# Performance work log

Measured on AMD Instinct MI355X. Metric: run time of the kernel, lower is better.

## Reference

```python
import jax, jax.numpy as jnp
import numpy as np

N_NODES = 50000
N_EDGES = 800000
IN_DIM = 128
HIDDEN = 32
HEADS = 4
OUT_DIM = 64
NEG_SLOPE = 0.2  # PyG GATConv default


def setup_inputs() -> dict:
    key = jax.random.key(0)
    ks = jax.random.split(key, 12)
    s = 0.05
    return {
        "x": jax.random.normal(ks[0], (N_NODES, IN_DIM), dtype=jnp.float32),
        "edge_index": jax.random.randint(ks[1], (2, N_EDGES), 0, N_NODES, dtype=jnp.int64),
        # layer 1: out = HEADS * HIDDEN, concat=True
        "W1": jax.random.normal(ks[2], (IN_DIM, HEADS * HIDDEN), dtype=jnp.float32) * s,
        "a_src1": jax.random.normal(ks[3], (HEADS, HIDDEN), dtype=jnp.float32) * s,
        "a_dst1": jax.random.normal(ks[4], (HEADS, HIDDEN), dtype=jnp.float32) * s,
        "b1": jnp.zeros((HEADS * HIDDEN,), dtype=jnp.float32),
        # layer 2: heads=1, concat=False
        "W2": jax.random.normal(ks[5], (HEADS * HIDDEN, OUT_DIM), dtype=jnp.float32) * s,
        "a_src2": jax.random.normal(ks[6], (1, OUT_DIM), dtype=jnp.float32) * s,
        "a_dst2": jax.random.normal(ks[7], (1, OUT_DIM), dtype=jnp.float32) * s,
        "b2": jnp.zeros((OUT_DIM,), dtype=jnp.float32),
    }


def _gat_conv(x, src, dst, W, a_src, a_dst, b, heads, concat):
    """PyG-style GATConv. src/dst already include self-loops."""
    N = x.shape[0]
    C = W.shape[1] // heads
    h = (x @ W).reshape(N, heads, C)              # [N,H,C]
    al_s = jnp.sum(h * a_src, axis=-1)            # [N,H]
    al_d = jnp.sum(h * a_dst, axis=-1)            # [N,H]
    e = jax.nn.leaky_relu(al_s[src] + al_d[dst], NEG_SLOPE)  # [E,H]
    # numerically-stable segment softmax over incoming edges of each dst node
    m = jax.ops.segment_max(e, dst, num_segments=N)          # [N,H]
    ex = jnp.exp(e - m[dst])
    denom = jax.ops.segment_sum(ex, dst, num_segments=N)     # [N,H]
    alpha = ex / denom[dst]                                   # [E,H]
    out = jax.ops.segment_sum(h[src] * alpha[:, :, None], dst, num_segments=N)  # [N,H,C]
    out = out.reshape(N, heads * C) if concat else out.mean(axis=1)
    return out + b


def reference(x, edge_index, W1, a_src1, a_dst1, b1, W2, a_src2, a_dst2, b2):
    N = x.shape[0]
    loop = jnp.arange(N, dtype=edge_index.dtype)
    src = jnp.concatenate([edge_index[0], loop])
    dst = jnp.concatenate([edge_index[1], loop])
    h = jax.nn.relu(_gat_conv(x, src, dst, W1, a_src1, a_dst1, b1, HEADS, True))
    out = _gat_conv(h, src, dst, W2, a_src2, a_dst2, b2, 1, False)
    return jax.nn.log_softmax(out, axis=1)
```

## Files before the change

kernel.cpp:

```cpp
#include <hip/hip_runtime.h>
#include <hip/hip_bf16.h>
#include <math.h>

#define N_NODES 50000
#define N_EDGES 800000
#define E_TOT   (N_EDGES + N_NODES)
#define IN_DIM  128
#define HID     128
#define ODIM    64
#define NEG     0.2f
#define NB1     ((N_NODES + 255) / 256)
#define NCHUNK  ((N_NODES + 31) / 32)
#define NREP    8

typedef short bf16x8 __attribute__((ext_vector_type(8)));
typedef float f32x4 __attribute__((ext_vector_type(4)));
typedef float f32x2 __attribute__((ext_vector_type(2)));
typedef unsigned short ushort_t;

__device__ __forceinline__ float lrelu(float x) { return x >= 0.f ? x : NEG * x; }

__device__ __forceinline__ unsigned short f2b(float v) {
  unsigned int b = __float_as_uint(v);
  b += 0x7fffu + ((b >> 16) & 1u);
  return (unsigned short)(b >> 16);
}
__device__ __forceinline__ float b2f(unsigned short u) {
  return __uint_as_float(((unsigned int)u) << 16);
}
__device__ __forceinline__ unsigned int f2b2(float lo, float hi) {
  union { __hip_bfloat162 h; unsigned int u; } cv;
  cv.h = __float22bfloat162_rn(make_float2(lo, hi));
  return cv.u;
}
__device__ __forceinline__ float blo(unsigned int v) { return __uint_as_float(v << 16); }
__device__ __forceinline__ float bhi(unsigned int v) { return __uint_as_float(v & 0xffff0000u); }

__device__ __forceinline__ f32x2 f8x2lo(unsigned int v) {
  return __builtin_amdgcn_cvt_pk_f32_fp8((int)v, false);
}
__device__ __forceinline__ f32x2 f8x2hi(unsigned int v) {
  return __builtin_amdgcn_cvt_pk_f32_fp8((int)v, true);
}
__device__ __forceinline__ unsigned char f2f8(float v) {
  return (unsigned char)(__builtin_amdgcn_cvt_pk_fp8_f32(v, v, 0, false) & 0xff);
}

__global__ void k_detect(const void* ei, int* flag) {
  if (threadIdx.x == 0 && blockIdx.x == 0) {
    const int* p = (const int*)ei;
    int allz = 1;
    for (int i = 0; i < 64; ++i) if (p[2 * i + 1] != 0) { allz = 0; break; }
    *flag = allz;
  }
}

__device__ __forceinline__ int e_src(const void* ei, int f, int e) {
  if (e >= N_EDGES) return e - N_EDGES;
  return f ? (int)((const long long*)ei)[e] : ((const int*)ei)[e];
}
__device__ __forceinline__ int e_dst(const void* ei, int f, int e) {
  if (e >= N_EDGES) return e - N_EDGES;
  return f ? (int)((const long long*)ei)[N_EDGES + e] : ((const int*)ei)[N_EDGES + e];
}

__global__ void k_hist(const void* ei, const int* flag, int* degr, int* rank) {
  int e = blockIdx.x * 256 + threadIdx.x;
  if (e >= E_TOT) return;
  int r = blockIdx.x & (NREP - 1);
  int d = e_dst(ei, *flag, e);
  rank[e] = atomicAdd(&degr[r * N_NODES + d], 1);
}

__global__ void k_scan1(const int* __restrict__ degr, int* __restrict__ offs, int* __restrict__ bsums) {
  __shared__ int sm[256];
  int t = threadIdx.x, i = blockIdx.x * 256 + t;
  int v = 0;
  if (i < N_NODES) {
    #pragma unroll
    for (int r = 0; r < NREP; ++r) v += degr[r * N_NODES + i];
  }
  sm[t] = v;
  __syncthreads();
  for (int o = 1; o < 256; o <<= 1) {
    int add = (t >= o) ? sm[t - o] : 0;
    __syncthreads();
    sm[t] += add;
    __syncthreads();
  }
  if (i < N_NODES) offs[i] = sm[t] - v;
  if (t == 255) bsums[blockIdx.x] = sm[255];
}

__global__ void k_scan2(int* bsums) {
  __shared__ int sm[256];
  int t = threadIdx.x;
  int v = (t < NB1) ? bsums[t] : 0;
  sm[t] = v;
  __syncthreads();
  for (int o = 1; o < 256; o <<= 1) {
    int add = (t >= o) ? sm[t - o] : 0;
    __syncthreads();
    sm[t] += add;
    __syncthreads();
  }
  if (t < NB1) bsums[t] = sm[t] - v;
}

__global__ void k_scan3(int* __restrict__ offs, const int* __restrict__ bsums,
                        const int* __restrict__ degr, int* __restrict__ repbase) {
  int i = blockIdx.x * 256 + threadIdx.x;
  if (i < N_NODES) {
    int o = offs[i] + bsums[blockIdx.x];
    offs[i] = o;
    int run = o;
    #pragma unroll
    for (int r = 0; r < NREP; ++r) {
      repbase[r * N_NODES + i] = run;
      run += degr[r * N_NODES + i];
    }
  }
  if (i == 0) offs[N_NODES] = E_TOT;
}

__global__ void k_scatter(const void* ei, const int* __restrict__ flag,
                          const int* __restrict__ repbase,
                          const int* __restrict__ rank, int* __restrict__ srcs) {
  int e = blockIdx.x * 256 + threadIdx.x;
  if (e >= E_TOT) return;
  int f = *flag;
  int d = e_dst(ei, f, e);
  int r = blockIdx.x & (NREP - 1);
  srcs[repbase[r * N_NODES + d] + rank[e]] = e_src(ei, f, e);
}

__global__ void k_prep(const float* __restrict__ W1, const float* __restrict__ W2,
                       ushort_t* __restrict__ Wt1, ushort_t* __restrict__ Wt2) {
  int i = blockIdx.x * 256 + threadIdx.x;
  if (i < 128 * 128) { int k = i >> 7, n = i & 127; Wt1[n * 128 + k] = f2b(W1[i]); }
  if (i < 128 * 64)  { int k = i >> 6, n = i & 63;  Wt2[n * 128 + k] = f2b(W2[i]); }
}

__global__ __launch_bounds__(256) void k_mm1(const float* __restrict__ x,
                                             const ushort_t* __restrict__ Wt,
                                             ushort_t* __restrict__ h1b,
                                             unsigned char* __restrict__ h1f8) {
  __shared__ ushort_t xs[32 * 128];
  int t = threadIdx.x;
  int w = t >> 6, l = t & 63;
  int lr = l & 15, lk = l >> 4;
  int nodeSub = (w & 1) * 16, colBase = (w >> 1) * 64;
  bf16x8 bfrag[4][4];
  #pragma unroll
  for (int ct = 0; ct < 4; ++ct)
    #pragma unroll
    for (int ks = 0; ks < 4; ++ks) {
      int n = colBase + ct * 16 + lr;
      int k = ks * 32 + lk * 8;
      bfrag[ct][ks] = *(const bf16x8*)&Wt[n * 128 + k];
    }
  int rr = t >> 3, c0 = (t & 7) * 16;
  for (int chunk = blockIdx.x; chunk < NCHUNK; chunk += gridDim.x) {
    int base = chunk * 32;
    int srcRow = base + rr; if (srcRow >= N_NODES) srcRow = N_NODES - 1;
    const float4* xr = (const float4*)&x[(size_t)srcRow * IN_DIM + c0];
    float4 f0 = xr[0], f1 = xr[1], f2 = xr[2], f3 = xr[3];
    uint4 w0, w1;
    w0.x = f2b2(f0.x, f0.y); w0.y = f2b2(f0.z, f0.w);
    w0.z = f2b2(f1.x, f1.y); w0.w = f2b2(f1.z, f1.w);
    w1.x = f2b2(f2.x, f2.y); w1.y = f2b2(f2.z, f2.w);
    w1.z = f2b2(f3.x, f3.y); w1.w = f2b2(f3.z, f3.w);
    char* xsb = (char*)xs;
    int swz = (rr & 7) << 4;
    *(uint4*)(xsb + rr * 256 + ((c0 * 2 +  0) ^ swz)) = w0;
    *(uint4*)(xsb + rr * 256 + ((c0 * 2 + 16) ^ swz)) = w1;
    __syncthreads();
    f32x4 acc[4] = {{0,0,0,0},{0,0,0,0},{0,0,0,0},{0,0,0,0}};
    int arow = nodeSub + lr;
    #pragma unroll
    for (int ks = 0; ks < 4; ++ks) {
      bf16x8 a = *(const bf16x8*)((const char*)xs + arow * 256 +
                                  ((ks * 64 + lk * 16) ^ ((arow & 7) << 4)));
      #pragma unroll
      for (int ct = 0; ct < 4; ++ct)
        acc[ct] = __builtin_amdgcn_mfma_f32_16x16x32_bf16(a, bfrag[ct][ks], acc[ct], 0, 0, 0);
    }
    __syncthreads();
    #pragma unroll
    for (int ct = 0; ct < 4; ++ct)
      #pragma unroll
      for (int r = 0; r < 4; ++r) {
        int node = base + nodeSub + lk * 4 + r;
        if (node < N_NODES) {
          float v = acc[ct][r];
          int col = colBase + ct * 16 + lr;
          h1b[(size_t)node * HID + col] = f2b(v);
          h1f8[(size_t)node * HID + col] = f2f8(v);
        }
      }
  }
}

__global__ __launch_bounds__(256) void k_mm2(const ushort_t* __restrict__ xb,
                                             const ushort_t* __restrict__ Wt,
                                             ushort_t* __restrict__ h2b,
                                             unsigned char* __restrict__ h2f8) {
  __shared__ ushort_t xs[32 * 128];
  int t = threadIdx.x;
  int w = t >> 6, l = t & 63;
  int lr = l & 15, lk = l >> 4;
  int nodeSub = (w & 1) * 16, colBase = (w >> 1) * 32;
  bf16x8 bfrag[2][4];
  #pragma unroll
  for (int ct = 0; ct < 2; ++ct)
    #pragma unroll
    for (int ks = 0; ks < 4; ++ks) {
      int n = colBase + ct * 16 + lr;
      int k = ks * 32 + lk * 8;
      bfrag[ct][ks] = *(const bf16x8*)&Wt[n * 128 + k];
    }
  int rr = t >> 3, c0 = (t & 7) * 16;
  for (int chunk = blockIdx.x; chunk < NCHUNK; chunk += gridDim.x) {
    int base = chunk * 32;
    int srcRow = base + rr; if (srcRow >= N_NODES) srcRow = N_NODES - 1;
    const uint4* xr = (const uint4*)&xb[(size_t)srcRow * HID + c0];
    uint4 w0 = xr[0], w1 = xr[1];
    char* xsb = (char*)xs;
    int swz = (rr & 7) << 4;
    *(uint4*)(xsb + rr * 256 + ((c0 * 2 +  0) ^ swz)) = w0;
    *(uint4*)(xsb + rr * 256 + ((c0 * 2 + 16) ^ swz)) = w1;
    __syncthreads();
    f32x4 acc[2] = {{0,0,0,0},{0,0,0,0}};
    int arow = nodeSub + lr;
    #pragma unroll
    for (int ks = 0; ks < 4; ++ks) {
      bf16x8 a = *(const bf16x8*)((const char*)xs + arow * 256 +
                                  ((ks * 64 + lk * 16) ^ ((arow & 7) << 4)));
      #pragma unroll
      for (int ct = 0; ct < 2; ++ct)
        acc[ct] = __builtin_amdgcn_mfma_f32_16x16x32_bf16(a, bfrag[ct][ks], acc[ct], 0, 0, 0);
    }
    __syncthreads();
    #pragma unroll
    for (int ct = 0; ct < 2; ++ct)
      #pragma unroll
      for (int r = 0; r < 4; ++r) {
        int node = base + nodeSub + lk * 4 + r;
        if (node < N_NODES) {
          float v = acc[ct][r];
          int col = colBase + ct * 16 + lr;
          h2b[(size_t)node * ODIM + col] = f2b(v);
          h2f8[(size_t)node * ODIM + col] = f2f8(v);
        }
      }
  }
}

__global__ __launch_bounds__(256) void k_al1(const ushort_t* __restrict__ h1b,
                                             const float* __restrict__ asrc,
                                             const float* __restrict__ adst, float* __restrict__ als,
                                             float* __restrict__ ald) {
  int t = threadIdx.x;
  int n = blockIdx.x * 16 + (t >> 4);
  int c8 = (t & 15) * 8;
  uint4 v = *(const uint4*)&h1b[(size_t)n * HID + c8];
  float4 a0 = *(const float4*)&asrc[c8], a1 = *(const float4*)&asrc[c8 + 4];
  float4 d0 = *(const float4*)&adst[c8], d1 = *(const float4*)&adst[c8 + 4];
  float f0 = blo(v.x), f1 = bhi(v.x), f2 = blo(v.y), f3 = bhi(v.y);
  float f4 = blo(v.z), f5 = bhi(v.z), f6 = blo(v.w), f7 = bhi(v.w);
  float s = f0*a0.x + f1*a0.y + f2*a0.z + f3*a0.w + f4*a1.x + f5*a1.y + f6*a1.z + f7*a1.w;
  float d = f0*d0.x + f1*d0.y + f2*d0.z + f3*d0.w + f4*d1.x + f5*d1.y + f6*d1.z + f7*d1.w;
  s += __shfl_xor(s, 1); s += __shfl_xor(s, 2);
  d += __shfl_xor(d, 1); d += __shfl_xor(d, 2);
  if ((t & 3) == 0) {
    int head = (t & 15) >> 2;
    als[n * 4 + head] = s;
    ald[n * 4 + head] = d;
  }
}

__global__ __launch_bounds__(256) void k_al2(const ushort_t* __restrict__ h2b,
                                             const float* __restrict__ asrc,
                                             const float* __restrict__ adst, float* __restrict__ als,
                                             float* __restrict__ ald) {
  int t = threadIdx.x;
  int n = blockIdx.x * 32 + (t >> 3);
  if (n >= N_NODES) return;
  int c8 = (t & 7) * 8;
  uint4 v = *(const uint4*)&h2b[(size_t)n * ODIM + c8];
  float4 a0 = *(const float4*)&asrc[c8], a1 = *(const float4*)&asrc[c8 + 4];
  float4 d0 = *(const float4*)&adst[c8], d1 = *(const float4*)&adst[c8 + 4];
  float f0 = blo(v.x), f1 = bhi(v.x), f2 = blo(v.y), f3 = bhi(v.y);
  float f4 = blo(v.z), f5 = bhi(v.z), f6 = blo(v.w), f7 = bhi(v.w);
  float s = f0*a0.x + f1*a0.y + f2*a0.z + f3*a0.w + f4*a1.x + f5*a1.y + f6*a1.z + f7*a1.w;
  float d = f0*d0.x + f1*d0.y + f2*d0.z + f3*d0.w + f4*d1.x + f5*d1.y + f6*d1.z + f7*d1.w;
  s += __shfl_xor(s, 1); s += __shfl_xor(s, 2); s += __shfl_xor(s, 4);
  d += __shfl_xor(d, 1); d += __shfl_xor(d, 2); d += __shfl_xor(d, 4);
  if ((t & 7) == 0) { als[n] = s; ald[n] = d; }
}

__global__ __launch_bounds__(256) void k_agg1(const unsigned char* __restrict__ h1f8,
                                              const float* __restrict__ als,
                                              const float* __restrict__ ald, const int* __restrict__ offs,
                                              const int* __restrict__ srcs, const float* __restrict__ b1,
                                              ushort_t* __restrict__ out1b) {
  int t = threadIdx.x;
  int w = t >> 6, l = t & 63;
  int eg = l >> 4, cl = l & 15, head = cl >> 2;
  int n = blockIdx.x * 4 + w;
  int off0 = offs[n], deg = offs[n + 1] - off0;
  const float4* als4 = (const float4*)als;
  float4 ad = ((const float4*)ald)[n];
  const unsigned char* hb = h1f8 + cl * 8;

  float ds = 0.f;
  float num0 = 0, num1 = 0, num2 = 0, num3 = 0, num4 = 0, num5 = 0, num6 = 0, num7 = 0;

  for (int cbase = 0; cbase < deg; cbase += 64) {
    int j0 = cbase + l;
    float w0 = 0.f, w1 = 0.f, w2 = 0.f, w3 = 0.f;
    int sb = 0;
    if (j0 < deg) {
      int s = srcs[off0 + j0];
      sb = s << 7;
      float4 a = als4[s];
      w0 = __expf(lrelu(a.x + ad.x)); w1 = __expf(lrelu(a.y + ad.y));
      w2 = __expf(lrelu(a.z + ad.z)); w3 = __expf(lrelu(a.w + ad.w));
    }
    int pw01 = (int)f2b2(w0, w1), pw23 = (int)f2b2(w2, w3);
    int cn = (deg - cbase) < 64 ? (deg - cbase) : 64;
    for (int jj = 0; jj < cn; jj += 8) {
      int jA = jj + eg, jB = jj + 4 + eg;
      int boA = __shfl(sb, jA), boB = __shfl(sb, jB);
      uint2 vA = *(const uint2*)(hb + boA);
      uint2 vB = *(const uint2*)(hb + boB);
      unsigned int uA01 = (unsigned int)__shfl(pw01, jA);
      unsigned int uA23 = (unsigned int)__shfl(pw23, jA);
      unsigned int uB01 = (unsigned int)__shfl(pw01, jB);
      unsigned int uB23 = (unsigned int)__shfl(pw23, jB);
      unsigned int upA = head < 2 ? uA01 : uA23;
      unsigned int upB = head < 2 ? uB01 : uB23;
      float wA = (head & 1) ? bhi(upA) : blo(upA);
      float wB = (head & 1) ? bhi(upB) : blo(upB);
      ds += wA + wB;
      f32x2 p0 = f8x2lo(vA.x), p1 = f8x2hi(vA.x);
      f32x2 p2 = f8x2lo(vA.y), p3 = f8x2hi(vA.y);
      num0 = fmaf(wA, p0.x, num0); num1 = fmaf(wA, p0.y, num1);
      num2 = fmaf(wA, p1.x, num2); num3 = fmaf(wA, p1.y, num3);
      num4 = fmaf(wA, p2.x, num4); num5 = fmaf(wA, p2.y, num5);
      num6 = fmaf(wA, p3.x, num6); num7 = fmaf(wA, p3.y, num7);
      p0 = f8x2lo(vB.x); p1 = f8x2hi(vB.x);
      p2 = f8x2lo(vB.y); p3 = f8x2hi(vB.y);
      num0 = fmaf(wB, p0.x, num0); num1 = fmaf(wB, p0.y, num1);
      num2 = fmaf(wB, p1.x, num2); num3 = fmaf(wB, p1.y, num3);
      num4 = fmaf(wB, p2.x, num4); num5 = fmaf(wB, p2.y, num5);
      num6 = fmaf(wB, p3.x, num6); num7 = fmaf(wB, p3.y, num7);
    }
  }
  #pragma unroll
  for (int o = 16; o <= 32; o <<= 1) {
    num0 += __shfl_xor(num0, o); num1 += __shfl_xor(num1, o);
    num2 += __shfl_xor(num2, o); num3 += __shfl_xor(num3, o);
    num4 += __shfl_xor(num4, o); num5 += __shfl_xor(num5, o);
    num6 += __shfl_xor(num6, o); num7 += __shfl_xor(num7, o);
    ds += __shfl_xor(ds, o);
  }
  if (l < 16) {
    float rd = 1.f / ds;
    int c8 = cl * 8;
    float4 bb0 = *(const float4*)&b1[c8];
    float4 bb1 = *(const float4*)&b1[c8 + 4];
    float o0 = fmaxf(num0 * rd + bb0.x, 0.f);
    float o1 = fmaxf(num1 * rd + bb0.y, 0.f);
    float o2 = fmaxf(num2 * rd + bb0.z, 0.f);
    float o3 = fmaxf(num3 * rd + bb0.w, 0.f);
    float o4 = fmaxf(num4 * rd + bb1.x, 0.f);
    float o5 = fmaxf(num5 * rd + bb1.y, 0.f);
    float o6 = fmaxf(num6 * rd + bb1.z, 0.f);
    float o7 = fmaxf(num7 * rd + bb1.w, 0.f);
    uint4 pk;
    pk.x = f2b2(o0, o1); pk.y = f2b2(o2, o3);
    pk.z = f2b2(o4, o5); pk.w = f2b2(o6, o7);
    *(uint4*)&out1b[(size_t)n * HID + c8] = pk;
  }
}

__global__ __launch_bounds__(256) void k_agg2(const unsigned char* __restrict__ h2f8,
                                              const float* __restrict__ als,
                                              const float* __restrict__ ald, const int* __restrict__ offs,
                                              const int* __restrict__ srcs, const float* __restrict__ b2,
                                              float* __restrict__ out) {
  int t = threadIdx.x;
  int w = t >> 6, l = t & 63;
  int eg = l >> 3, cl = l & 7;
  int n = blockIdx.x * 4 + w;
  int off0 = offs[n], deg = offs[n + 1] - off0;
  float adv = ald[n];
  const unsigned char* hb = h2f8 + cl * 8;

  float ds = 0.f;
  float num0 = 0, num1 = 0, num2 = 0, num3 = 0, num4 = 0, num5 = 0, num6 = 0, num7 = 0;

  for (int cbase = 0; cbase < deg; cbase += 64) {
    int j0 = cbase + l;
    float wv = 0.f;
    int sb = 0;
    if (j0 < deg) {
      int s = srcs[off0 + j0];
      sb = s << 6;
      wv = __expf(lrelu(als[s] + adv));
    }
    int cn = (deg - cbase) < 64 ? (deg - cbase) : 64;
    for (int jj = 0; jj < cn; jj += 16) {
      int jA = jj + eg, jB = jj + 8 + eg;
      int boA = __shfl(sb, jA), boB = __shfl(sb, jB);
      uint2 vA = *(const uint2*)(hb + boA);
      uint2 vB = *(const uint2*)(hb + boB);
      float wA = __shfl(wv, jA), wB = __shfl(wv, jB);
      ds += wA + wB;
      f32x2 p0 = f8x2lo(vA.x), p1 = f8x2hi(vA.x);
      f32x2 p2 = f8x2lo(vA.y), p3 = f8x2hi(vA.y);
      num0 = fmaf(wA, p0.x, num0); num1 = fmaf(wA, p0.y, num1);
      num2 = fmaf(wA, p1.x, num2); num3 = fmaf(wA, p1.y, num3);
      num4 = fmaf(wA, p2.x, num4); num5 = fmaf(wA, p2.y, num5);
      num6 = fmaf(wA, p3.x, num6); num7 = fmaf(wA, p3.y, num7);
      p0 = f8x2lo(vB.x); p1 = f8x2hi(vB.x);
      p2 = f8x2lo(vB.y); p3 = f8x2hi(vB.y);
      num0 = fmaf(wB, p0.x, num0); num1 = fmaf(wB, p0.y, num1);
      num2 = fmaf(wB, p1.x, num2); num3 = fmaf(wB, p1.y, num3);
      num4 = fmaf(wB, p2.x, num4); num5 = fmaf(wB, p2.y, num5);
      num6 = fmaf(wB, p3.x, num6); num7 = fmaf(wB, p3.y, num7);
    }
  }
  #pragma unroll
  for (int o = 8; o <= 32; o <<= 1) {
    num0 += __shfl_xor(num0, o); num1 += __shfl_xor(num1, o);
    num2 += __shfl_xor(num2, o); num3 += __shfl_xor(num3, o);
    num4 += __shfl_xor(num4, o); num5 += __shfl_xor(num5, o);
    num6 += __shfl_xor(num6, o); num7 += __shfl_xor(num7, o);
    ds += __shfl_xor(ds, o);
  }
  if (l < 8) {
    float rd = 1.f / ds;
    int c8 = cl * 8;
    float4 bb0 = *(const float4*)&b2[c8];
    float4 bb1 = *(const float4*)&b2[c8 + 4];
    float v0 = num0 * rd + bb0.x, v1 = num1 * rd + bb0.y;
    float v2 = num2 * rd + bb0.z, v3 = num3 * rd + bb0.w;
    float v4 = num4 * rd + bb1.x, v5 = num5 * rd + bb1.y;
    float v6 = num6 * rd + bb1.z, v7 = num7 * rd + bb1.w;
    float mx = fmaxf(fmaxf(fmaxf(v0, v1), fmaxf(v2, v3)), fmaxf(fmaxf(v4, v5), fmaxf(v6, v7)));
    #pragma unroll
    for (int o = 1; o <= 4; o <<= 1) mx = fmaxf(mx, __shfl_xor(mx, o));
    float sum = __expf(v0 - mx) + __expf(v1 - mx) + __expf(v2 - mx) + __expf(v3 - mx)
              + __expf(v4 - mx) + __expf(v5 - mx) + __expf(v6 - mx) + __expf(v7 - mx);
    #pragma unroll
    for (int o = 1; o <= 4; o <<= 1) sum += __shfl_xor(sum, o);
    float ls = __logf(sum);
    float4 r0, r1;
    r0.x = (v0 - mx) - ls; r0.y = (v1 - mx) - ls; r0.z = (v2 - mx) - ls; r0.w = (v3 - mx) - ls;
    r1.x = (v4 - mx) - ls; r1.y = (v5 - mx) - ls; r1.z = (v6 - mx) - ls; r1.w = (v7 - mx) - ls;
    *(float4*)&out[(size_t)n * ODIM + c8] = r0;
    *(float4*)&out[(size_t)n * ODIM + c8 + 4] = r1;
  }
}

extern "C" void kernel_launch(void* const* d_in, const int* in_sizes, int n_in,
                              void* d_out, int out_size, void* d_ws, size_t ws_size,
                              hipStream_t stream) {
  const float* x   = (const float*)d_in[0];
  const void*  ei  = d_in[1];
  const float* W1  = (const float*)d_in[2];
  const float* as1 = (const float*)d_in[3];
  const float* ad1 = (const float*)d_in[4];
  const float* b1  = (const float*)d_in[5];
  const float* W2  = (const float*)d_in[6];
  const float* as2 = (const float*)d_in[7];
  const float* ad2 = (const float*)d_in[8];
  const float* b2  = (const float*)d_in[9];
  float* out = (float*)d_out;

  char* ws = (char*)d_ws;
  size_t o = 0;
  auto alloc = [&](size_t bytes) { void* p = (void*)(ws + o); o += (bytes + 255) & ~(size_t)255; return p; };
  ushort_t* h1b   = (ushort_t*)alloc((size_t)N_NODES * HID * 2);
  ushort_t* out1b = (ushort_t*)alloc((size_t)N_NODES * HID * 2);
  ushort_t* h2b   = (ushort_t*)alloc((size_t)N_NODES * ODIM * 2);
  unsigned char* h1f8 = (unsigned char*)alloc((size_t)N_NODES * HID);
  ushort_t* Wt1   = (ushort_t*)alloc((size_t)128 * 128 * 2);
  ushort_t* Wt2   = (ushort_t*)alloc((size_t)64 * 128 * 2);
  float* als1 = (float*)alloc((size_t)N_NODES * 4 * 4);
  float* ald1 = (float*)alloc((size_t)N_NODES * 4 * 4);
  float* als2 = (float*)alloc((size_t)N_NODES * 4);
  float* ald2 = (float*)alloc((size_t)N_NODES * 4);
  int*   degr = (int*)alloc((size_t)NREP * N_NODES * 4);
  int*   repbase = (int*)alloc((size_t)NREP * N_NODES * 4);
  int*   offs = (int*)alloc((size_t)(N_NODES + 1) * 4);
  int*   rank = (int*)alloc((size_t)E_TOT * 4);
  int*   srcs = (int*)alloc((size_t)E_TOT * 4);
  int*   bsums= (int*)alloc((size_t)NB1 * 4);
  int*   flag = (int*)alloc(4);
  unsigned char* h2f8 = (unsigned char*)rank;

  hipMemsetAsync(degr, 0, (size_t)NREP * N_NODES * 4, stream);
  k_detect<<<1, 64, 0, stream>>>(ei, flag);

  int egrid = (E_TOT + 255) / 256;
  k_hist   <<<egrid, 256, 0, stream>>>(ei, flag, degr, rank);
  k_scan1  <<<NB1,   256, 0, stream>>>(degr, offs, bsums);
  k_scan2  <<<1,     256, 0, stream>>>(bsums);
  k_scan3  <<<NB1,   256, 0, stream>>>(offs, bsums, degr, repbase);
  k_scatter<<<egrid, 256, 0, stream>>>(ei, flag, repbase, rank, srcs);
  k_prep   <<<64,    256, 0, stream>>>(W1, W2, Wt1, Wt2);

  k_mm1  <<<512, 256, 0, stream>>>(x, Wt1, h1b, h1f8);
  k_al1  <<<N_NODES / 16, 256, 0, stream>>>(h1b, as1, ad1, als1, ald1);
  k_agg1 <<<(N_NODES + 3) / 4, 256, 0, stream>>>(h1f8, als1, ald1, offs, srcs, b1, out1b);

  k_mm2  <<<512, 256, 0, stream>>>(out1b, Wt2, h2b, h2f8);
  k_al2  <<<(N_NODES + 31) / 32, 256, 0, stream>>>(h2b, as2, ad2, als2, ald2);
  k_agg2 <<<(N_NODES + 3) / 4, 256, 0, stream>>>(h2f8, als2, ald2, offs, srcs, b2, out);
}
```

Before: 148.6 us.

## Map two nodes per wavefront in aggregation kernels and fold detect into prep

Both edge-aggregation kernels now give each destination node a 32-lane half-wave instead of a full 64-lane wave. Edge chunks are therefore 32 wide and the shuffles are offset into the matching half. The aim is to stop wasting lanes on low-degree nodes, since average degree is about 17, and to halve the block count. The separate int32/int64 index-detect kernel is merged into k_prep as an extra block, saving one launch and moving weight prep earlier. The trade-off is fewer lanes in flight per edge for high-degree nodes, so more loop iterations there.

```diff
diff --git a/kernel.cpp b/kernel.cpp
--- a/kernel.cpp
+++ b/kernel.cpp
@@ -46,15 +46,6 @@
   return (unsigned char)(__builtin_amdgcn_cvt_pk_fp8_f32(v, v, 0, false) & 0xff);
 }
 
-__global__ void k_detect(const void* ei, int* flag) {
-  if (threadIdx.x == 0 && blockIdx.x == 0) {
-    const int* p = (const int*)ei;
-    int allz = 1;
-    for (int i = 0; i < 64; ++i) if (p[2 * i + 1] != 0) { allz = 0; break; }
-    *flag = allz;
-  }
-}
-
 __device__ __forceinline__ int e_src(const void* ei, int f, int e) {
   if (e >= N_EDGES) return e - N_EDGES;
   return f ? (int)((const long long*)ei)[e] : ((const int*)ei)[e];
@@ -62,6 +53,23 @@
 __device__ __forceinline__ int e_dst(const void* ei, int f, int e) {
   if (e >= N_EDGES) return e - N_EDGES;
   return f ? (int)((const long long*)ei)[N_EDGES + e] : ((const int*)ei)[N_EDGES + e];
+}
+
+__global__ void k_prep(const float* __restrict__ W1, const float* __restrict__ W2,
+                       ushort_t* __restrict__ Wt1, ushort_t* __restrict__ Wt2,
+                       const void* ei, int* flag) {
+  if (blockIdx.x == 64) {
+    if (threadIdx.x == 0) {
+      const int* p = (const int*)ei;
+      int allz = 1;
+      for (int i = 0; i < 64; ++i) if (p[2 * i + 1] != 0) { allz = 0; break; }
+      *flag = allz;
+    }
+    return;
+  }
+  int i = blockIdx.x * 256 + threadIdx.x;
+  if (i < 128 * 128) { int k = i >> 7, n = i & 127; Wt1[n * 128 + k] = f2b(W1[i]); }
+  if (i < 128 * 64)  { int k = i >> 6, n = i & 63;  Wt2[n * 128 + k] = f2b(W2[i]); }
 }
 
 __global__ void k_hist(const void* ei, const int* flag, int* degr, int* rank) {
@@ -132,13 +140,6 @@
   int d = e_dst(ei, f, e);
   int r = blockIdx.x & (NREP - 1);
   srcs[repbase[r * N_NODES + d] + rank[e]] = e_src(ei, f, e);
-}
-
-__global__ void k_prep(const float* __restrict__ W1, const float* __restrict__ W2,
-                       ushort_t* __restrict__ Wt1, ushort_t* __restrict__ Wt2) {
-  int i = blockIdx.x * 256 + threadIdx.x;
-  if (i < 128 * 128) { int k = i >> 7, n = i & 127; Wt1[n * 128 + k] = f2b(W1[i]); }
-  if (i < 128 * 64)  { int k = i >> 6, n = i & 63;  Wt2[n * 128 + k] = f2b(W2[i]); }
 }
 
 __global__ __launch_bounds__(256) void k_mm1(const float* __restrict__ x,
@@ -306,8 +307,10 @@
                                               ushort_t* __restrict__ out1b) {
   int t = threadIdx.x;
   int w = t >> 6, l = t & 63;
-  int eg = l >> 4, cl = l & 15, head = cl >> 2;
-  int n = blockIdx.x * 4 + w;
+  int hw = l >> 5, lh = l & 31;
+  int sg = lh >> 4, cl = lh & 15, head = cl >> 2;
+  int lbase = hw << 5;
+  int n = blockIdx.x * 8 + w * 2 + hw;
   int off0 = offs[n], deg = offs[n + 1] - off0;
   const float4* als4 = (const float4*)als;
   float4 ad = ((const float4*)ald)[n];
@@ -316,8 +319,8 @@
   float ds = 0.f;
   float num0 = 0, num1 = 0, num2 = 0, num3 = 0, num4 = 0, num5 = 0, num6 = 0, num7 = 0;
 
-  for (int cbase = 0; cbase < deg; cbase += 64) {
-    int j0 = cbase + l;
+  for (int cbase = 0; cbase < deg; cbase += 32) {
+    int j0 = cbase + lh;
     float w0 = 0.f, w1 = 0.f, w2 = 0.f, w3 = 0.f;
     int sb = 0;
     if (j0 < deg) {
@@ -328,16 +331,16 @@
       w2 = __expf(lrelu(a.z + ad.z)); w3 = __expf(lrelu(a.w + ad.w));
     }
     int pw01 = (int)f2b2(w0, w1), pw23 = (int)f2b2(w2, w3);
-    int cn = (deg - cbase) < 64 ? (deg - cbase) : 64;
-    for (int jj = 0; jj < cn; jj += 8) {
-      int jA = jj + eg, jB = jj + 4 + eg;
-      int boA = __shfl(sb, jA), boB = __shfl(sb, jB);
+    int cn = (deg - cbase) < 32 ? (deg - cbase) : 32;
+    for (int jj = 0; jj < cn; jj += 4) {
+      int jA = jj + sg, jB = jj + 2 + sg;
+      int boA = __shfl(sb, lbase + jA), boB = __shfl(sb, lbase + jB);
       uint2 vA = *(const uint2*)(hb + boA);
       uint2 vB = *(const uint2*)(hb + boB);
-      unsigned int uA01 = (unsigned int)__shfl(pw01, jA);
-      unsigned int uA23 = (unsigned int)__shfl(pw23, jA);
-      unsigned int uB01 = (unsigned int)__shfl(pw01, jB);
-      unsigned int uB23 = (unsigned int)__shfl(pw23, jB);
+      unsigned int uA01 = (unsigned int)__shfl(pw01, lbase + jA);
+      unsigned int uA23 = (unsigned int)__shfl(pw23, lbase + jA);
+      unsigned int uB01 = (unsigned int)__shfl(pw01, lbase + jB);
+      unsigned int uB23 = (unsigned int)__shfl(pw23, lbase + jB);
       unsigned int upA = head < 2 ? uA01 : uA23;
       unsigned int upB = head < 2 ? uB01 : uB23;
       float wA = (head & 1) ? bhi(upA) : blo(upA);
@@ -357,15 +360,12 @@
       num6 = fmaf(wB, p3.x, num6); num7 = fmaf(wB, p3.y, num7);
     }
   }
-  #pragma unroll
-  for (int o = 16; o <= 32; o <<= 1) {
-    num0 += __shfl_xor(num0, o); num1 += __shfl_xor(num1, o);
-    num2 += __shfl_xor(num2, o); num3 += __shfl_xor(num3, o);
-    num4 += __shfl_xor(num4, o); num5 += __shfl_xor(num5, o);
-    num6 += __shfl_xor(num6, o); num7 += __shfl_xor(num7, o);
-    ds += __shfl_xor(ds, o);
-  }
-  if (l < 16) {
+  num0 += __shfl_xor(num0, 16); num1 += __shfl_xor(num1, 16);
+  num2 += __shfl_xor(num2, 16); num3 += __shfl_xor(num3, 16);
+  num4 += __shfl_xor(num4, 16); num5 += __shfl_xor(num5, 16);
+  num6 += __shfl_xor(num6, 16); num7 += __shfl_xor(num7, 16);
+  ds += __shfl_xor(ds, 16);
+  if (lh < 16) {
     float rd = 1.f / ds;
     int c8 = cl * 8;
     float4 bb0 = *(const float4*)&b1[c8];
@@ -392,8 +392,10 @@
                                               float* __restrict__ out) {
   int t = threadIdx.x;
   int w = t >> 6, l = t & 63;
-  int eg = l >> 3, cl = l & 7;
-  int n = blockIdx.x * 4 + w;
+  int hw = l >> 5, lh = l & 31;
+  int sg = lh >> 3, cl = lh & 7;
+  int lbase = hw << 5;
+  int n = blockIdx.x * 8 + w * 2 + hw;
   int off0 = offs[n], deg = offs[n + 1] - off0;
   float adv = ald[n];
   const unsigned char* hb = h2f8 + cl * 8;
@@ -401,8 +403,8 @@
   float ds = 0.f;
   float num0 = 0, num1 = 0, num2 = 0, num3 = 0, num4 = 0, num5 = 0, num6 = 0, num7 = 0;
 
-  for (int cbase = 0; cbase < deg; cbase += 64) {
-    int j0 = cbase + l;
+  for (int cbase = 0; cbase < deg; cbase += 32) {
+    int j0 = cbase + lh;
     float wv = 0.f;
     int sb = 0;
     if (j0 < deg) {
@@ -410,13 +412,13 @@
       sb = s << 6;
       wv = __expf(lrelu(als[s] + adv));
     }
-    int cn = (deg - cbase) < 64 ? (deg - cbase) : 64;
-    for (int jj = 0; jj < cn; jj += 16) {
-      int jA = jj + eg, jB = jj + 8 + eg;
-      int boA = __shfl(sb, jA), boB = __shfl(sb, jB);
+    int cn = (deg - cbase) < 32 ? (deg - cbase) : 32;
+    for (int jj = 0; jj < cn; jj += 8) {
+      int jA = jj + sg, jB = jj + 4 + sg;
+      int boA = __shfl(sb, lbase + jA), boB = __shfl(sb, lbase + jB);
       uint2 vA = *(const uint2*)(hb + boA);
       uint2 vB = *(const uint2*)(hb + boB);
-      float wA = __shfl(wv, jA), wB = __shfl(wv, jB);
+      float wA = __shfl(wv, lbase + jA), wB = __shfl(wv, lbase + jB);
       ds += wA + wB;
       f32x2 p0 = f8x2lo(vA.x), p1 = f8x2hi(vA.x);
       f32x2 p2 = f8x2lo(vA.y), p3 = f8x2hi(vA.y);
@@ -433,14 +435,14 @@
     }
   }
   #pragma unroll
-  for (int o = 8; o <= 32; o <<= 1) {
+  for (int o = 8; o <= 16; o <<= 1) {
     num0 += __shfl_xor(num0, o); num1 += __shfl_xor(num1, o);
     num2 += __shfl_xor(num2, o); num3 += __shfl_xor(num3, o);
     num4 += __shfl_xor(num4, o); num5 += __shfl_xor(num5, o);
     num6 += __shfl_xor(num6, o); num7 += __shfl_xor(num7, o);
     ds += __shfl_xor(ds, o);
   }
-  if (l < 8) {
+  if (lh < 8) {
     float rd = 1.f / ds;
     int c8 = cl * 8;
     float4 bb0 = *(const float4*)&b2[c8];
@@ -503,7 +505,7 @@
   unsigned char* h2f8 = (unsigned char*)rank;
 
   hipMemsetAsync(degr, 0, (size_t)NREP * N_NODES * 4, stream);
-  k_detect<<<1, 64, 0, stream>>>(ei, flag);
+  k_prep   <<<65,    256, 0, stream>>>(W1, W2, Wt1, Wt2, ei, flag);
 
   int egrid = (E_TOT + 255) / 256;
   k_hist   <<<egrid, 256, 0, stream>>>(ei, flag, degr, rank);
@@ -511,13 +513,12 @@
   k_scan2  <<<1,     256, 0, stream>>>(bsums);
   k_scan3  <<<NB1,   256, 0, stream>>>(offs, bsums, degr, repbase);
   k_scatter<<<egrid, 256, 0, stream>>>(ei, flag, repbase, rank, srcs);
-  k_prep   <<<64,    256, 0, stream>>>(W1, W2, Wt1, Wt2);
 
   k_mm1  <<<512, 256, 0, stream>>>(x, Wt1, h1b, h1f8);
   k_al1  <<<N_NODES / 16, 256, 0, stream>>>(h1b, as1, ad1, als1, ald1);
-  k_agg1 <<<(N_NODES + 3) / 4, 256, 0, stream>>>(h1f8, als1, ald1, offs, srcs, b1, out1b);
+  k_agg1 <<<N_NODES / 8, 256, 0, stream>>>(h1f8, als1, ald1, offs, srcs, b1, out1b);
 
   k_mm2  <<<512, 256, 0, stream>>>(out1b, Wt2, h2b, h2f8);
   k_al2  <<<(N_NODES + 31) / 32, 256, 0, stream>>>(h2b, as2, ad2, als2, ald2);
-  k_agg2 <<<(N_NODES + 3) / 4, 256, 0, stream>>>(h2f8, als2, ald2, offs, srcs, b2, out);
-}
+  k_agg2 <<<N_NODES / 8, 256, 0, stream>>>(h2f8, als2, ald2, offs, srcs, b2, out);
+}
```

Result: faster. 134.3 us (-9.6%).
